# Kernel optimization log

Hardware: AMD Instinct MI355X
Metric: run time of the kernel (lower is better)

## Reference

```python
import jax, jax.numpy as jnp
import numpy as np

B, S, E = 2, 2048, 1024          # batch, seq, emb_size
H, D = 16, 64                     # heads, head_dim
NE, K = 8, 2                      # num_experts, top_k


def setup_inputs() -> dict:
    key = jax.random.key(0)
    ks = jax.random.split(key, 12)
    w = lambda k, shape: jax.random.normal(k, shape, jnp.float32) * 0.02
    return {
        "x": jax.random.normal(ks[0], (B, S, E), jnp.float32),
        "q_w": w(ks[1], (E, E)), "q_b": jnp.zeros((E,), jnp.float32),
        "k_w": w(ks[2], (E, E)), "k_b": jnp.zeros((E,), jnp.float32),
        "v_w": w(ks[3], (E, E)), "v_b": jnp.zeros((E,), jnp.float32),
        "gate_w": w(ks[4], (NE, E)), "gate_b": jnp.zeros((NE,), jnp.float32),
        "expert_w": w(ks[5], (NE, E, E)), "expert_b": jnp.zeros((NE, E), jnp.float32),
        "ffn_w": w(ks[6], (E, E)), "ffn_b": jnp.zeros((E,), jnp.float32),
    }


def _rope_cos_sin(seq_len, dim):
    inv_freq = 1.0 / (10000.0 ** (jnp.arange(0, dim, 2, dtype=jnp.float32) / dim))
    freqs = jnp.outer(jnp.arange(seq_len, dtype=jnp.float32), inv_freq)  # [S, D/2]
    emb = jnp.concatenate([freqs, freqs], axis=-1)                        # [S, D]
    return jnp.cos(emb), jnp.sin(emb)


def _rotate_half(x):
    x1, x2 = jnp.split(x, 2, axis=-1)
    return jnp.concatenate([-x2, x1], axis=-1)


def reference(x, q_w, q_b, k_w, k_b, v_w, v_b, gate_w, gate_b, expert_w, expert_b, ffn_w, ffn_b):
    b, s, _ = x.shape
    q = (x @ q_w.T + q_b).reshape(b, s, H, D)
    k = (x @ k_w.T + k_b).reshape(b, s, H, D)
    v = (x @ v_w.T + v_b).reshape(b, s, H, D)

    cos, sin = _rope_cos_sin(s, D)          # [S, D]
    cos = cos[None, :, None, :]
    sin = sin[None, :, None, :]
    q = q * cos + _rotate_half(q) * sin
    k = k * cos + _rotate_half(k) * sin

    # full (memory-efficient-style) attention, scale 1/sqrt(D)
    scores = jnp.einsum('bqhd,bkhd->bhqk', q, k) / jnp.sqrt(jnp.float32(D))
    attn = jax.nn.softmax(scores, axis=-1)
    attn_out = jnp.einsum('bhqk,bkhd->bqhd', attn, v).reshape(b, s, E)

    # MoE: dense-compute all experts, gather top-k, weighted combine
    gates = jax.nn.softmax(attn_out @ gate_w.T + gate_b, axis=-1)        # [B,S,NE]
    top_gates, top_idx = jax.lax.top_k(gates, K)                          # [B,S,K]
    # Linear per expert: y = x W^T + b,  expert_w: [NE, out, in]
    expert_outputs = jnp.einsum('bsi,noi->bsno', attn_out, expert_w) + expert_b  # [B,S,NE,E]
    sel = jnp.take_along_axis(expert_outputs, top_idx[..., None], axis=2)        # [B,S,K,E]
    moe_out = jnp.einsum('bsk,bskh->bsh', top_gates, sel)                        # [B,S,E]

    # dropout is identity at inference; ffn + residual
    return moe_out @ ffn_w.T + ffn_b + x
```

## Files before the change

### kernel.cpp

```cpp
#include <hip/hip_runtime.h>
#include <hip/hip_bf16.h>

#define B_ 2
#define S_ 2048
#define E_ 1024
#define H_ 16
#define D_ 64
#define NE_ 8
#define TOKENS (B_*S_)

typedef __attribute__((ext_vector_type(8))) short bf16x8;
typedef __attribute__((ext_vector_type(4))) float f32x4;
typedef unsigned short u16;
typedef unsigned int u32;

__device__ __forceinline__ u16 f2bf(float f) {
    u32 u = __float_as_uint(f);
    u32 r = u + 0x7fffu + ((u >> 16) & 1u);
    return (u16)(r >> 16);
}
__device__ __forceinline__ float bf2f(u16 h) {
    return __uint_as_float(((u32)h) << 16);
}
__device__ __forceinline__ void gl2lds16(const void* g, void* l) {
    __builtin_amdgcn_global_load_lds(
        (__attribute__((address_space(1))) void*)(g),
        (__attribute__((address_space(3))) void*)(l), 16, 0, 0);
}
#define MFMA16(a,b,c) __builtin_amdgcn_mfma_f32_16x16x32_bf16(a,b,c,0,0,0)

__global__ void cvt_all_k(
    const float* __restrict__ x,  const float* __restrict__ qw,
    const float* __restrict__ kw, const float* __restrict__ vw,
    const float* __restrict__ fw, const float* __restrict__ ew,
    u16* __restrict__ xh,  u16* __restrict__ qwh, u16* __restrict__ kwh,
    u16* __restrict__ vwh, u16* __restrict__ fwh, u16* __restrict__ ewh)
{
    const int blk = blockIdx.x;
    const float* s; u16* d; int off;
    if (blk < 4096)      { s = x;  d = xh;  off = blk; }
    else if (blk < 5120) { s = qw; d = qwh; off = blk - 4096; }
    else if (blk < 6144) { s = kw; d = kwh; off = blk - 5120; }
    else if (blk < 7168) { s = vw; d = vwh; off = blk - 6144; }
    else if (blk < 8192) { s = fw; d = fwh; off = blk - 7168; }
    else                 { s = ew; d = ewh; off = blk - 8192; }
    const size_t i = (size_t)off * 256 + threadIdx.x;
    const float4 v = *(const float4*)(s + i * 4);
    ushort4 H = {f2bf(v.x), f2bf(v.y), f2bf(v.z), f2bf(v.w)};
    *(ushort4*)(d + i * 4) = H;
}

__global__ void rope_tab_kernel(float2* __restrict__ tab)
{
    const int idx = blockIdx.x * 256 + threadIdx.x;
    const int s = idx >> 5, d1 = idx & 31;
    const float inv = exp2f(-(float)d1 * 0.41524101186091903f);
    float sn, cs;
    sincosf((float)s * inv, &sn, &cs);
    tab[idx] = make_float2(cs, sn);
}

__global__ __launch_bounds__(256,2) void gemm_qkv(
    const u16* __restrict__ Ah,
    const u16* __restrict__ qwh, const u16* __restrict__ kwh,
    const u16* __restrict__ vwh,
    const float* __restrict__ q_b, const float* __restrict__ k_b,
    const float* __restrict__ v_b,
    const float2* __restrict__ tab,
    u16* __restrict__ Qhb, u16* __restrict__ Khb, u16* __restrict__ Vtb)
{
    __shared__ __align__(16) u16 sA[128*32], sB[128*32];
    const int z = blockIdx.z;
    const u16* Bh = (z == 0) ? qwh : (z == 1) ? kwh : vwh;
    const float* bias = (z == 0) ? q_b : (z == 1) ? k_b : v_b;
    const int t = threadIdx.x;
    const int m0 = blockIdx.y * 128, n0 = blockIdx.x * 128;
    const int lane = t & 63, w = t >> 6;
    const int wm = w >> 1, wn = w & 1;
    const int lr = lane & 15, qd = lane >> 4;
    f32x4 acc[4][4] = {};
    const size_t gA = (size_t)(m0 + (t >> 2)) * E_ + (t & 3) * 8;
    const size_t gB = (size_t)(n0 + (t >> 2)) * E_ + (t & 3) * 8;
    for (int k0 = 0; k0 < E_; k0 += 32) {
        #pragma unroll
        for (int is = 0; is < 2; is++) {
            const int ldo = (is * 256 + (t & 192)) * 16;
            const size_t ro = (size_t)is * 64 * E_;
            gl2lds16(Ah + gA + ro + k0, (char*)sA + ldo);
            gl2lds16(Bh + gB + ro + k0, (char*)sB + ldo);
        }
        __syncthreads();
        bf16x8 af[4], bfr[4];
        #pragma unroll
        for (int i = 0; i < 4; i++) {
            af[i]  = *(const bf16x8*)&sA[(wm*64 + i*16 + lr)*32 + qd*8];
            bfr[i] = *(const bf16x8*)&sB[(wn*64 + i*16 + lr)*32 + qd*8];
        }
        #pragma unroll
        for (int i = 0; i < 4; i++)
            #pragma unroll
            for (int j = 0; j < 4; j++)
                acc[i][j] = MFMA16(af[i], bfr[j], acc[i][j]);
        __syncthreads();
    }
    const int head = (n0 + wn * 64) >> 6;
    if (z < 2) {
        u16* Oh = (z == 0) ? Qhb : Khb;
        #pragma unroll
        for (int j = 0; j < 2; j++) {
            const int d1 = j * 16 + lr;
            const float b1 = bias[head * 64 + d1];
            const float b2 = bias[head * 64 + d1 + 32];
            #pragma unroll
            for (int i = 0; i < 4; i++) {
                #pragma unroll
                for (int r = 0; r < 4; r++) {
                    const int tok = m0 + wm*64 + i*16 + qd*4 + r;
                    const int bb = tok >> 11, ss = tok & (S_ - 1);
                    const float2 t2 = tab[ss * 32 + d1];
                    const float q1 = acc[i][j][r]   + b1;
                    const float q2 = acc[i][j+2][r] + b2;
                    const size_t o = (((size_t)bb * H_ + head) * S_ + ss) * 64 + d1;
                    Oh[o]    = f2bf(q1 * t2.x - q2 * t2.y);
                    Oh[o+32] = f2bf(q2 * t2.x + q1 * t2.y);
                }
            }
        }
    } else {
        #pragma unroll
        for (int j = 0; j < 4; j++) {
            const int d = j * 16 + lr;
            const float bv = bias[head * 64 + d];
            #pragma unroll
            for (int i = 0; i < 4; i++)
                #pragma unroll
                for (int r = 0; r < 4; r++) {
                    const int tok = m0 + wm*64 + i*16 + qd*4 + r;
                    const int bb = tok >> 11, ss = tok & (S_ - 1);
                    Vtb[(((size_t)bb * H_ + head) * 64 + d) * S_ + ss] = f2bf(acc[i][j][r] + bv);
                }
        }
    }
}

__global__ __launch_bounds__(256,4) void attn_kernel(
    const u16* __restrict__ Q, const u16* __restrict__ K,
    const u16* __restrict__ Vt,
    float* __restrict__ Opart, float* __restrict__ lpart)
{
    __shared__ __align__(16) u16 sK[64*64];
    __shared__ __align__(16) u16 sV[64*64];
    __shared__ __align__(16) u16 sP[4][2][16*40];
    const int t = threadIdx.x, lane = t & 63, w = t >> 6;
    const int lr = lane & 15, qd = lane >> 4;
    const int q0 = blockIdx.x * 128;
    const int h = blockIdx.y;
    const int b = blockIdx.z & 1, sc = blockIdx.z >> 1;
    const size_t bhS = ((size_t)b * H_ + h) * S_;
    const size_t bhD = ((size_t)b * H_ + h) * 64;
    bf16x8 qf[2][2];
    #pragma unroll
    for (int p = 0; p < 2; p++) {
        const size_t qa = (bhS + q0 + p*64 + w*16 + lr) * 64 + qd * 8;
        qf[p][0] = *(const bf16x8*)&Q[qa];
        qf[p][1] = *(const bf16x8*)&Q[qa + 32];
    }
    f32x4 O[2][4] = {};
    float lsum[2][4] = {};
    const int jbeg = sc * 1024, jend = jbeg + 1024;
    for (int j0 = jbeg; j0 < jend; j0 += 64) {
        #pragma unroll
        for (int it = 0; it < 2; it++) {
            const int CH = (it*4 + w)*4 + qd;
            const int sbs = CH >> 3;
            const int doff = ((CH >> 2) & 1)*32 + (CH & 3)*8;
            gl2lds16(&K [(bhS + j0 + sbs*16 + lr)*64 + doff],
                     (char*)sK + (it*4 + w)*1024);
            gl2lds16(&Vt[(bhD + sbs*16 + lr)*S_ + j0 + doff],
                     (char*)sV + (it*4 + w)*1024);
        }
        __syncthreads();
        {
            f32x4 Sv[2][4];
            #pragma unroll
            for (int sb = 0; sb < 4; sb++) {
                bf16x8 k0 = *(const bf16x8*)&sK[(sb*8 + qd)*128 + lr*8];
                bf16x8 k1 = *(const bf16x8*)&sK[(sb*8 + 4 + qd)*128 + lr*8];
                f32x4 a0 = {}, a1 = {};
                a0 = MFMA16(qf[0][0], k0, a0);
                a0 = MFMA16(qf[0][1], k1, a0);
                a1 = MFMA16(qf[1][0], k0, a1);
                a1 = MFMA16(qf[1][1], k1, a1);
                Sv[0][sb] = a0;
                Sv[1][sb] = a1;
            }
            #pragma unroll
            for (int p = 0; p < 2; p++) {
                float ps[4] = {};
                #pragma unroll
                for (int sb = 0; sb < 4; sb++)
                    #pragma unroll
                    for (int r = 0; r < 4; r++) {
                        const float pv = __expf(Sv[p][sb][r] * 0.125f);
                        ps[r] += pv;
                        sP[w][p][(qd*4 + r)*40 + sb*16 + lr] = f2bf(pv);
                    }
                #pragma unroll
                for (int r = 0; r < 4; r++) lsum[p][r] += ps[r];
            }
        }
        {
            bf16x8 vv[8];
            #pragma unroll
            for (int ds = 0; ds < 4; ds++) {
                vv[2*ds]   = *(const bf16x8*)&sV[(ds*8 + qd)*128 + lr*8];
                vv[2*ds+1] = *(const bf16x8*)&sV[(ds*8 + 4 + qd)*128 + lr*8];
            }
            #pragma unroll
            for (int p = 0; p < 2; p++) {
                bf16x8 p0 = *(const bf16x8*)&sP[w][p][lr*40 + qd*8];
                bf16x8 p1 = *(const bf16x8*)&sP[w][p][lr*40 + 32 + qd*8];
                #pragma unroll
                for (int ds = 0; ds < 4; ds++) {
                    O[p][ds] = MFMA16(p0, vv[2*ds],   O[p][ds]);
                    O[p][ds] = MFMA16(p1, vv[2*ds+1], O[p][ds]);
                }
            }
        }
        __syncthreads();
    }
    float* Op = Opart + (size_t)sc * TOKENS * E_;
    float* lp = lpart + (size_t)sc * TOKENS * H_;
    #pragma unroll
    for (int p = 0; p < 2; p++) {
        #pragma unroll
        for (int r = 0; r < 4; r++) {
            float s2 = lsum[p][r];
            s2 += __shfl_xor(s2, 1, 64);
            s2 += __shfl_xor(s2, 2, 64);
            s2 += __shfl_xor(s2, 4, 64);
            s2 += __shfl_xor(s2, 8, 64);
            lsum[p][r] = s2;
        }
        const int qb = q0 + p*64 + w*16 + qd*4;
        if (lr == 0) {
            #pragma unroll
            for (int r = 0; r < 4; r++)
                lp[(size_t)(b*S_ + qb + r) * H_ + h] = lsum[p][r];
        }
        #pragma unroll
        for (int ds = 0; ds < 4; ds++)
            #pragma unroll
            for (int r = 0; r < 4; r++)
                Op[(size_t)(b*S_ + qb + r) * E_ + h*64 + ds*16 + lr] = O[p][ds][r];
    }
}

__global__ __launch_bounds__(256) void combine_gate(
    const float* __restrict__ Opart, const float* __restrict__ lpart,
    const float* __restrict__ gate_w, const float* __restrict__ gate_b,
    u16* __restrict__ attn_bf, float* __restrict__ gval, int* __restrict__ eidx)
{
    __shared__ float red[4][NE_];
    __shared__ float lg8[NE_];
    const int tok = blockIdx.x;
    const int t = threadIdx.x;
    const int d4 = t * 4;
    const int h = d4 >> 6;
    const float l = lpart[(size_t)tok*H_ + h] + lpart[(size_t)(TOKENS + tok)*H_ + h];
    const float inv = 1.f / l;
    const float4 o1 = *(const float4*)&Opart[(size_t)tok*E_ + d4];
    const float4 o2 = *(const float4*)&Opart[(size_t)(TOKENS + tok)*E_ + d4];
    float v[4] = {(o1.x+o2.x)*inv, (o1.y+o2.y)*inv, (o1.z+o2.z)*inv, (o1.w+o2.w)*inv};
    ushort4 H4 = {f2bf(v[0]), f2bf(v[1]), f2bf(v[2]), f2bf(v[3])};
    *(ushort4*)&attn_bf[(size_t)tok*E_ + d4] = H4;
    float pe[NE_];
    #pragma unroll
    for (int e = 0; e < NE_; e++) {
        const float4 g = *(const float4*)&gate_w[e*E_ + d4];
        pe[e] = v[0]*g.x + v[1]*g.y + v[2]*g.z + v[3]*g.w;
    }
    #pragma unroll
    for (int e = 0; e < NE_; e++) {
        #pragma unroll
        for (int off = 32; off >= 1; off >>= 1)
            pe[e] += __shfl_xor(pe[e], off, 64);
    }
    const int w = t >> 6;
    if ((t & 63) == 0) {
        #pragma unroll
        for (int e = 0; e < NE_; e++) red[w][e] = pe[e];
    }
    __syncthreads();
    if (t < NE_)
        lg8[t] = red[0][t] + red[1][t] + red[2][t] + red[3][t] + gate_b[t];
    __syncthreads();
    if (t == 0) {
        float lg[NE_];
        #pragma unroll
        for (int e = 0; e < NE_; e++) lg[e] = lg8[e];
        float m = lg[0];
        #pragma unroll
        for (int e = 1; e < NE_; e++) m = fmaxf(m, lg[e]);
        float ex[NE_], ssum = 0.f;
        #pragma unroll
        for (int e = 0; e < NE_; e++) { ex[e] = __expf(lg[e]-m); ssum += ex[e]; }
        const float invs = 1.f / ssum;
        int i0 = 0;
        #pragma unroll
        for (int e = 1; e < NE_; e++) if (lg[e] > lg[i0]) i0 = e;
        int i1 = (i0 == 0) ? 1 : 0;
        #pragma unroll
        for (int e = 0; e < NE_; e++) if (e != i0 && lg[e] > lg[i1]) i1 = e;
        eidx[tok*2]     = i0;
        gval[tok*2]     = ex[i0]*invs;
        eidx[tok*2 + 1] = i1;
        gval[tok*2 + 1] = ex[i1]*invs;
    }
}

__global__ __launch_bounds__(256) void build_lists_kernel(
    const int* __restrict__ eidx, int* __restrict__ list, int* __restrict__ counts)
{
    __shared__ int lcnt[NE_], lbase[NE_];
    const int t = threadIdx.x;
    if (t < NE_) lcnt[t] = 0;
    __syncthreads();
    const int ent = blockIdx.x * 512 + t * 2;
    const int e0 = eidx[ent], e1 = eidx[ent + 1];
    const int p0 = atomicAdd(&lcnt[e0], 1);
    const int p1 = atomicAdd(&lcnt[e1], 1);
    __syncthreads();
    if (t < NE_) lbase[t] = atomicAdd(&counts[t], lcnt[t]);
    __syncthreads();
    list[e0 * TOKENS + lbase[e0] + p0] = ent;
    list[e1 * TOKENS + lbase[e1] + p1] = ent + 1;
}

__global__ __launch_bounds__(256,2) void gemm_expert(
    const u16* __restrict__ Abf, const u16* __restrict__ ewh,
    const float* __restrict__ eb, const int* __restrict__ list,
    const int* __restrict__ counts, const float* __restrict__ gval,
    u16* __restrict__ sel)
{
    const int e = blockIdx.z;
    const int cnt = counts[e];
    const int m0 = blockIdx.y * 128;
    if (m0 >= cnt) return;
    __shared__ __align__(16) u16 sA[128*32], sB[128*32];
    __shared__ int sEnt[128];
    const int t = threadIdx.x;
    if (t < 128) sEnt[t] = (m0 + t < cnt) ? list[e * TOKENS + m0 + t] : -1;
    __syncthreads();
    const int n0 = blockIdx.x * 128;
    const int lane = t & 63, w = t >> 6;
    const int wm = w >> 1, wn = w & 1;
    const int lr = lane & 15, qd = lane >> 4;
    const int e0 = sEnt[t >> 2], e1 = sEnt[64 + (t >> 2)];
    const u16* ga0 = Abf + (size_t)(e0 < 0 ? 0 : (e0 >> 1)) * E_ + (t & 3) * 8;
    const u16* ga1 = Abf + (size_t)(e1 < 0 ? 0 : (e1 >> 1)) * E_ + (t & 3) * 8;
    const u16* gb0 = ewh + (size_t)e * E_ * E_ + (size_t)(n0 + (t >> 2)) * E_ + (t & 3) * 8;
    const u16* gb1 = gb0 + 64 * E_;
    f32x4 acc[4][4] = {};
    for (int k0 = 0; k0 < E_; k0 += 32) {
        {
            const int l0 = (t & 192) * 16;
            const int l1 = (256 + (t & 192)) * 16;
            gl2lds16(ga0 + k0, (char*)sA + l0);
            gl2lds16(ga1 + k0, (char*)sA + l1);
            gl2lds16(gb0 + k0, (char*)sB + l0);
            gl2lds16(gb1 + k0, (char*)sB + l1);
        }
        __syncthreads();
        bf16x8 af[4], bfr[4];
        #pragma unroll
        for (int i = 0; i < 4; i++) {
            af[i]  = *(const bf16x8*)&sA[(wm*64 + i*16 + lr)*32 + qd*8];
            bfr[i] = *(const bf16x8*)&sB[(wn*64 + i*16 + lr)*32 + qd*8];
        }
        #pragma unroll
        for (int i = 0; i < 4; i++)
            #pragma unroll
            for (int j = 0; j < 4; j++)
                acc[i][j] = MFMA16(af[i], bfr[j], acc[i][j]);
        __syncthreads();
    }
    #pragma unroll
    for (int i = 0; i < 4; i++)
        #pragma unroll
        for (int r = 0; r < 4; r++) {
            const int local = wm*64 + i*16 + qd*4 + r;
            const int ent = sEnt[local];
            if (ent < 0) continue;
            const float g = gval[ent];
            #pragma unroll
            for (int j = 0; j < 4; j++) {
                const int col = n0 + wn*64 + j*16 + lr;
                sel[(size_t)ent * E_ + col] = f2bf((acc[i][j][r] + eb[e * E_ + col]) * g);
            }
        }
}

__global__ void combine_kernel(const u16* __restrict__ sel, u16* __restrict__ moe)
{
    const int g = blockIdx.x * 256 + threadIdx.x;
    const int tok = g >> 8;
    const int c = (g & 255) * 4;
    const u16* a = sel + (size_t)tok * 2048 + c;
    float o[4];
    #pragma unroll
    for (int j = 0; j < 4; j++) o[j] = bf2f(a[j]) + bf2f(a[1024 + j]);
    ushort4 R = {f2bf(o[0]), f2bf(o[1]), f2bf(o[2]), f2bf(o[3])};
    *(ushort4*)(moe + (size_t)tok * E_ + c) = R;
}

__global__ __launch_bounds__(256,2) void gemm_ffn(
    const u16* __restrict__ Ah, const u16* __restrict__ Bh,
    const float* __restrict__ bias, const float* __restrict__ res,
    float* __restrict__ C)
{
    __shared__ __align__(16) u16 sA[128*32], sB[128*32];
    const int t = threadIdx.x;
    const int m0 = blockIdx.y * 128, n0 = blockIdx.x * 128;
    const int lane = t & 63, w = t >> 6;
    const int wm = w >> 1, wn = w & 1;
    const int lr = lane & 15, qd = lane >> 4;
    f32x4 acc[4][4] = {};
    const size_t gA = (size_t)(m0 + (t >> 2)) * E_ + (t & 3) * 8;
    const size_t gB = (size_t)(n0 + (t >> 2)) * E_ + (t & 3) * 8;
    for (int k0 = 0; k0 < E_; k0 += 32) {
        #pragma unroll
        for (int is = 0; is < 2; is++) {
            const int ldo = (is * 256 + (t & 192)) * 16;
            const size_t ro = (size_t)is * 64 * E_;
            gl2lds16(Ah + gA + ro + k0, (char*)sA + ldo);
            gl2lds16(Bh + gB + ro + k0, (char*)sB + ldo);
        }
        __syncthreads();
        bf16x8 af[4], bfr[4];
        #pragma unroll
        for (int i = 0; i < 4; i++) {
            af[i]  = *(const bf16x8*)&sA[(wm*64 + i*16 + lr)*32 + qd*8];
            bfr[i] = *(const bf16x8*)&sB[(wn*64 + i*16 + lr)*32 + qd*8];
        }
        #pragma unroll
        for (int i = 0; i < 4; i++)
            #pragma unroll
            for (int j = 0; j < 4; j++)
                acc[i][j] = MFMA16(af[i], bfr[j], acc[i][j]);
        __syncthreads();
    }
    #pragma unroll
    for (int i = 0; i < 4; i++)
        #pragma unroll
        for (int r = 0; r < 4; r++) {
            const int tok = m0 + wm*64 + i*16 + qd*4 + r;
            #pragma unroll
            for (int j = 0; j < 4; j++) {
                const int col = n0 + wn*64 + j*16 + lr;
                C[(size_t)tok * E_ + col] = acc[i][j][r] + bias[col] + res[(size_t)tok * E_ + col];
            }
        }
}

extern "C" void kernel_launch(void* const* d_in, const int* in_sizes, int n_in,
                              void* d_out, int out_size, void* d_ws, size_t ws_size,
                              hipStream_t stream) {
    const float* x      = (const float*)d_in[0];
    const float* q_w    = (const float*)d_in[1];
    const float* q_b    = (const float*)d_in[2];
    const float* k_w    = (const float*)d_in[3];
    const float* k_b    = (const float*)d_in[4];
    const float* v_w    = (const float*)d_in[5];
    const float* v_b    = (const float*)d_in[6];
    const float* gate_w = (const float*)d_in[7];
    const float* gate_b = (const float*)d_in[8];
    const float* ew     = (const float*)d_in[9];
    const float* eb     = (const float*)d_in[10];
    const float* ffn_w  = (const float*)d_in[11];
    const float* ffn_b  = (const float*)d_in[12];
    float* out = (float*)d_out;

    char* p = (char*)d_ws;
    auto alloc = [&](size_t bytes) { char* r = p; p += (bytes + 255) & ~(size_t)255; return r; };
    u16* xh   = (u16*)alloc((size_t)TOKENS*E_*2);
    u16* qwh  = (u16*)alloc((size_t)E_*E_*2);
    u16* kwh  = (u16*)alloc((size_t)E_*E_*2);
    u16* vwh  = (u16*)alloc((size_t)E_*E_*2);
    u16* fwh  = (u16*)alloc((size_t)E_*E_*2);
    u16* ewh  = (u16*)alloc((size_t)NE_*E_*E_*2);
    u16* Qhb  = (u16*)alloc((size_t)TOKENS*E_*2);
    u16* Khb  = (u16*)alloc((size_t)TOKENS*E_*2);
    u16* Vtb  = (u16*)alloc((size_t)TOKENS*E_*2);
    u16* abf  = (u16*)alloc((size_t)TOKENS*E_*2);
    float* Opart = (float*)alloc((size_t)2*TOKENS*E_*4);
    float* lpart = (float*)alloc((size_t)2*TOKENS*H_*4);
    u16* selb = (u16*)alloc((size_t)2*TOKENS*E_*2);
    u16* moeb = (u16*)alloc((size_t)TOKENS*E_*2);
    float2* rtab = (float2*)alloc((size_t)S_*32*8);
    float* gvl = (float*)alloc((size_t)2*TOKENS*4);
    int*   eix = (int*)alloc((size_t)2*TOKENS*4);
    int*   lst = (int*)alloc((size_t)NE_*TOKENS*4);
    int*   cnt = (int*)alloc(256);

    hipMemsetAsync(cnt, 0, 256, stream);

    rope_tab_kernel<<<S_*32/256, 256, 0, stream>>>(rtab);
    cvt_all_k<<<16384, 256, 0, stream>>>(x, q_w, k_w, v_w, ffn_w, ew,
                                         xh, qwh, kwh, vwh, fwh, ewh);

    gemm_qkv<<<dim3(8,32,3), 256, 0, stream>>>(xh, qwh, kwh, vwh,
                                               q_b, k_b, v_b, rtab,
                                               Qhb, Khb, Vtb);

    attn_kernel<<<dim3(16,16,4), 256, 0, stream>>>(Qhb, Khb, Vtb, Opart, lpart);

    combine_gate<<<TOKENS, 256, 0, stream>>>(Opart, lpart, gate_w, gate_b,
                                             abf, gvl, eix);
    build_lists_kernel<<<TOKENS/256, 256, 0, stream>>>(eix, lst, cnt);
    gemm_expert<<<dim3(8,32,8), 256, 0, stream>>>(abf, ewh, eb, lst, cnt, gvl, selb);
    combine_kernel<<<4096, 256, 0, stream>>>(selb, moeb);
    gemm_ffn<<<dim3(8,32), 256, 0, stream>>>(moeb, fwh, ffn_b, x, out);
}
```

Measured before the change: 304.4 us.

## Fold softmax scale into Q, transpose score MFMA, pack bf16 P stores

```diff
diff --git a/kernel.cpp b/kernel.cpp
--- a/kernel.cpp
+++ b/kernel.cpp
@@ -8,6 +8,7 @@
 #define D_ 64
 #define NE_ 8
 #define TOKENS (B_*S_)
+#define QSCALE 0.18033688011112043f
 
 typedef __attribute__((ext_vector_type(8))) short bf16x8;
 typedef __attribute__((ext_vector_type(4))) float f32x4;
@@ -106,6 +107,7 @@
     const int head = (n0 + wn * 64) >> 6;
     if (z < 2) {
         u16* Oh = (z == 0) ? Qhb : Khb;
+        const float osc = (z == 0) ? QSCALE : 1.0f;
         #pragma unroll
         for (int j = 0; j < 2; j++) {
             const int d1 = j * 16 + lr;
@@ -121,8 +123,8 @@
                     const float q1 = acc[i][j][r]   + b1;
                     const float q2 = acc[i][j+2][r] + b2;
                     const size_t o = (((size_t)bb * H_ + head) * S_ + ss) * 64 + d1;
-                    Oh[o]    = f2bf(q1 * t2.x - q2 * t2.y);
-                    Oh[o+32] = f2bf(q2 * t2.x + q1 * t2.y);
+                    Oh[o]    = f2bf((q1 * t2.x - q2 * t2.y) * osc);
+                    Oh[o+32] = f2bf((q2 * t2.x + q1 * t2.y) * osc);
                 }
             }
         }
@@ -166,7 +168,7 @@
         qf[p][1] = *(const bf16x8*)&Q[qa + 32];
     }
     f32x4 O[2][4] = {};
-    float lsum[2][4] = {};
+    float lsum[2] = {};
     const int jbeg = sc * 1024, jend = jbeg + 1024;
     for (int j0 = jbeg; j0 < jend; j0 += 64) {
         #pragma unroll
@@ -180,34 +182,37 @@
                      (char*)sV + (it*4 + w)*1024);
         }
         __syncthreads();
-        {
-            f32x4 Sv[2][4];
+        f32x4 Sv[2][4];
+        #pragma unroll
+        for (int sb = 0; sb < 4; sb++) {
+            bf16x8 k0 = *(const bf16x8*)&sK[(sb*8 + qd)*128 + lr*8];
+            bf16x8 k1 = *(const bf16x8*)&sK[(sb*8 + 4 + qd)*128 + lr*8];
+            f32x4 a0 = {}, a1 = {};
+            a0 = MFMA16(k0, qf[0][0], a0);
+            a0 = MFMA16(k1, qf[0][1], a0);
+            a1 = MFMA16(k0, qf[1][0], a1);
+            a1 = MFMA16(k1, qf[1][1], a1);
+            Sv[0][sb] = a0;
+            Sv[1][sb] = a1;
+        }
+        #pragma unroll
+        for (int p = 0; p < 2; p++) {
+            float ps = 0.f;
             #pragma unroll
             for (int sb = 0; sb < 4; sb++) {
-                bf16x8 k0 = *(const bf16x8*)&sK[(sb*8 + qd)*128 + lr*8];
-                bf16x8 k1 = *(const bf16x8*)&sK[(sb*8 + 4 + qd)*128 + lr*8];
-                f32x4 a0 = {}, a1 = {};
-                a0 = MFMA16(qf[0][0], k0, a0);
-                a0 = MFMA16(qf[0][1], k1, a0);
-                a1 = MFMA16(qf[1][0], k0, a1);
-                a1 = MFMA16(qf[1][1], k1, a1);
-                Sv[0][sb] = a0;
-                Sv[1][sb] = a1;
+                const float pv0 = exp2f(Sv[p][sb][0]);
+                const float pv1 = exp2f(Sv[p][sb][1]);
+                const float pv2 = exp2f(Sv[p][sb][2]);
+                const float pv3 = exp2f(Sv[p][sb][3]);
+                ps += (pv0 + pv1) + (pv2 + pv3);
+                const u32 w0 = (__float_as_uint(pv0) >> 16) |
+                               (__float_as_uint(pv1) & 0xffff0000u);
+                const u32 w1 = (__float_as_uint(pv2) >> 16) |
+                               (__float_as_uint(pv3) & 0xffff0000u);
+                uint2 pk; pk.x = w0; pk.y = w1;
+                *(uint2*)&sP[w][p][lr*40 + sb*16 + qd*4] = pk;
             }
-            #pragma unroll
-            for (int p = 0; p < 2; p++) {
-                float ps[4] = {};
-                #pragma unroll
-                for (int sb = 0; sb < 4; sb++)
-                    #pragma unroll
-                    for (int r = 0; r < 4; r++) {
-                        const float pv = __expf(Sv[p][sb][r] * 0.125f);
-                        ps[r] += pv;
-                        sP[w][p][(qd*4 + r)*40 + sb*16 + lr] = f2bf(pv);
-                    }
-                #pragma unroll
-                for (int r = 0; r < 4; r++) lsum[p][r] += ps[r];
-            }
+            lsum[p] += ps;
         }
         {
             bf16x8 vv[8];
@@ -233,21 +238,19 @@
     float* lp = lpart + (size_t)sc * TOKENS * H_;
     #pragma unroll
     for (int p = 0; p < 2; p++) {
-        #pragma unroll
-        for (int r = 0; r < 4; r++) {
-            float s2 = lsum[p][r];
-            s2 += __shfl_xor(s2, 1, 64);
-            s2 += __shfl_xor(s2, 2, 64);
-            s2 += __shfl_xor(s2, 4, 64);
-            s2 += __shfl_xor(s2, 8, 64);
-            lsum[p][r] = s2;
-        }
+        float s2 = lsum[p];
+        s2 += __shfl_xor(s2, 16, 64);
+        s2 += __shfl_xor(s2, 32, 64);
+        lsum[p] = s2;
+    }
+    if (lane < 16) {
+        #pragma unroll
+        for (int p = 0; p < 2; p++)
+            lp[(size_t)(b*S_ + q0 + p*64 + w*16 + lane) * H_ + h] = lsum[p];
+    }
+    #pragma unroll
+    for (int p = 0; p < 2; p++) {
         const int qb = q0 + p*64 + w*16 + qd*4;
-        if (lr == 0) {
-            #pragma unroll
-            for (int r = 0; r < 4; r++)
-                lp[(size_t)(b*S_ + qb + r) * H_ + h] = lsum[p][r];
-        }
         #pragma unroll
         for (int ds = 0; ds < 4; ds++)
             #pragma unroll
```

Result: no change. 307.2 us (+0.9%).
